# Kernel optimization log

Measured on AMD Instinct MI355X. Metric: run time of the kernel, lower is better.

Reference implementation:

```python
import jax, jax.numpy as jnp
import numpy as np

NEG_SLOPE = 0.2

def _gat_conv(x, src, dst, W, att_src, att_dst, bias, num_nodes):
    # x: [N, Fin], W: [H*C, Fin], att_*: [H, C], bias: [H*C]
    H, C = att_src.shape
    xh = (x @ W.T).reshape(num_nodes, H, C)            # [N,H,C]
    a_s = jnp.einsum('nhc,hc->nh', xh, att_src)         # [N,H]
    a_d = jnp.einsum('nhc,hc->nh', xh, att_dst)
    e = jax.nn.leaky_relu(a_s[src] + a_d[dst], NEG_SLOPE)  # [E,H]
    # segment softmax over destination node per head
    m = jax.ops.segment_max(e, dst, num_segments=num_nodes)      # [N,H]
    ex = jnp.exp(e - m[dst])
    s = jax.ops.segment_sum(ex, dst, num_segments=num_nodes)     # [N,H]
    alpha = ex / (s[dst] + 1e-16)                                # [E,H]
    msg = xh[src] * alpha[:, :, None]                            # [E,H,C]
    out = jax.ops.segment_sum(msg, dst, num_segments=num_nodes)  # [N,H,C]
    return out.reshape(num_nodes, H * C) + bias


def setup_inputs() -> dict:
    key = jax.random.key(0)
    ks = jax.random.split(key, 16)
    N, E, Fin, Hd, H1, G = 50000, 800000, 128, 128, 4, 128
    x = jax.random.normal(ks[0], (N, Fin), dtype=jnp.float32)
    edge_index = jax.random.randint(ks[1], (2, E), 0, N, dtype=jnp.int64)
    batch = jnp.sort(jax.random.randint(ks[2], (N,), 0, G, dtype=jnp.int64))
    sc1 = 1.0 / np.sqrt(Fin)
    sc2 = 1.0 / np.sqrt(Hd * H1)
    sch = 1.0 / np.sqrt(Hd)
    return {
        'x': x, 'edge_index': edge_index, 'batch': batch,
        'W1': jax.random.normal(ks[3], (Hd * H1, Fin), dtype=jnp.float32) * sc1,
        'as1': jax.random.normal(ks[4], (H1, Hd), dtype=jnp.float32) * 0.1,
        'ad1': jax.random.normal(ks[5], (H1, Hd), dtype=jnp.float32) * 0.1,
        'b1': jnp.zeros((Hd * H1,), dtype=jnp.float32),
        'W2': jax.random.normal(ks[6], (Hd, Hd * H1), dtype=jnp.float32) * sc2,
        'as2': jax.random.normal(ks[7], (1, Hd), dtype=jnp.float32) * 0.1,
        'ad2': jax.random.normal(ks[8], (1, Hd), dtype=jnp.float32) * 0.1,
        'b2': jnp.zeros((Hd,), dtype=jnp.float32),
        'Wh1': jax.random.normal(ks[9], (Hd, Hd), dtype=jnp.float32) * sch,
        'bh1': jnp.zeros((Hd,), dtype=jnp.float32),
        'Wh2': jax.random.normal(ks[10], (1, Hd), dtype=jnp.float32) * sch,
        'bh2': jnp.zeros((1,), dtype=jnp.float32),
    }


def reference(x, edge_index, batch, W1, as1, ad1, b1, W2, as2, ad2, b2, Wh1, bh1, Wh2, bh2):
    N = x.shape[0]
    G = 128  # num graphs
    # add self loops (PyG GATConv default)
    loops = jnp.arange(N, dtype=edge_index.dtype)
    src = jnp.concatenate([edge_index[0], loops])
    dst = jnp.concatenate([edge_index[1], loops])
    h = _gat_conv(x, src, dst, W1, as1, ad1, b1, N)   # [N, 512]
    h = jax.nn.elu(h)
    h = _gat_conv(h, src, dst, W2, as2, ad2, b2, N)   # [N, 128]
    h = jax.nn.elu(h)
    # global mean pool over batch
    sums = jax.ops.segment_sum(h, batch, num_segments=G)
    cnts = jax.ops.segment_sum(jnp.ones((N,), dtype=h.dtype), batch, num_segments=G)
    pooled = sums / jnp.maximum(cnts, 1.0)[:, None]   # [G, 128]
    z = jax.nn.relu(pooled @ Wh1.T + bh1)
    out = z @ Wh2.T + bh2                             # [G, 1]
    return out.reshape(-1)
```

## Files before the change

### kernel.cpp

```cpp
#include <hip/hip_runtime.h>
#include <cstdint>
#include <cstddef>

#define NEG_SLOPE 0.2f

typedef _Float16 f16x8 __attribute__((ext_vector_type(8)));
typedef _Float16 f16x2 __attribute__((ext_vector_type(2)));
typedef float    f32x4 __attribute__((ext_vector_type(4)));
typedef float    f32x2 __attribute__((ext_vector_type(2)));

__device__ __forceinline__ float leaky(float x){ return x > 0.f ? x : NEG_SLOPE * x; }
__device__ __forceinline__ float elu(float x){ return x > 0.f ? x : __expf(x) - 1.f; }

__global__ __launch_bounds__(256) void k_prep(const float* __restrict__ W1,
                                              const float* __restrict__ W2,
                                              const float* __restrict__ as1,
                                              const float* __restrict__ ad1,
                                              _Float16* __restrict__ W1hi, _Float16* __restrict__ W1lo,
                                              _Float16* __restrict__ W2hi, _Float16* __restrict__ W2lo,
                                              float* __restrict__ w_s, float* __restrict__ w_d)
{
    int b = blockIdx.x;
    if (b < 512) {
        const float* src = (b < 256) ? W1 : W2;
        _Float16* hi = (b < 256) ? W1hi : W2hi;
        _Float16* lo = (b < 256) ? W1lo : W2lo;
        int i = ((b & 255) << 8) + threadIdx.x;
        float v = src[i];
        _Float16 h = (_Float16)v;
        hi[i] = h;
        lo[i] = (_Float16)(v - (float)h);
    } else {
        int h = (b - 512) * 2 + (threadIdx.x >> 7);
        int k = threadIdx.x & 127;
        float s = 0.f, d = 0.f;
        for (int c = 0; c < 128; ++c) {
            float w = W1[((size_t)(h * 128 + c)) * 128 + k];
            s += as1[h * 128 + c] * w;
            d += ad1[h * 128 + c] * w;
        }
        w_s[h * 128 + k] = s;
        w_d[h * 128 + k] = d;
    }
}

#define LSG 40
#define CP  136
template<bool FUSE_BIAS_ELU, bool FUSE_ATTN2>
__global__ __launch_bounds__(256, 2) void k_gemm_h(
    const _Float16* __restrict__ A, const _Float16* __restrict__ Bh,
    const _Float16* __restrict__ Bl, const float* __restrict__ bias,
    _Float16* __restrict__ C,
    const float* __restrict__ as2, const float* __restrict__ ad2,
    float* __restrict__ As2, float* __restrict__ Ad2,
    int M, int K, int lda, int ldb, int ldc,
    long aZ, long bZ, long cZ, long biasZ)
{
    __shared__ __align__(16) _Float16 smem[128 * CP];
    _Float16* As  = smem;
    _Float16* Bhs = smem + 128 * LSG;
    _Float16* Bls = smem + 256 * LSG;

    const _Float16* Ab  = A  + (size_t)blockIdx.z * aZ;
    const _Float16* Bhb = Bh + (size_t)blockIdx.z * bZ;
    const _Float16* Blb = Bl + (size_t)blockIdx.z * bZ;
    _Float16* Cb = C + (size_t)blockIdx.z * cZ;

    const int tid = threadIdx.x;
    const int wave = tid >> 6, lane = tid & 63;
    const int wm = wave >> 1, wn = wave & 1;
    const int quad = lane >> 4, l16 = lane & 15;
    const int m0 = blockIdx.x * 128;

    f32x4 acc[4][4] = {};

    for (int k0 = 0; k0 < K; k0 += 32) {
// ... 42 lines not shown
                if (FUSE_BIAS_ELU) v = elu(v + bb);
                smem[(wm * 64 + i * 16 + quad * 4 + r) * CP + n] = (_Float16)v;
            }
    }
    __syncthreads();
    for (int c = tid; c < 2048; c += 256) {
        int row = c >> 4, col8 = (c & 15) * 8;
        int m = m0 + row;
        if (m < M)
            *(f16x8*)(Cb + (size_t)m * ldc + col8) = *(const f16x8*)&smem[row * CP + col8];
    }
    if (FUSE_ATTN2) {
        int row = tid >> 1, half = tid & 1;
        int d = m0 + row;
        float ss = 0.f, sd = 0.f;
        const _Float16* rp = &smem[row * CP + half * 64];
        #pragma unroll
        for (int c8 = 0; c8 < 8; ++c8) {
            f16x8 v = *(const f16x8*)(rp + c8 * 8);
            #pragma unroll
            for (int c = 0; c < 8; ++c) {
                float f = (float)v[c];
                int n = half * 64 + c8 * 8 + c;
                ss += f * as2[n];
                sd += f * ad2[n];
            }
        }
        ss += __shfl_xor(ss, 1);
        sd += __shfl_xor(sd, 1);
        if (half == 0 && d < M) { As2[d] = ss; Ad2[d] = sd; }
    }
}

__global__ __launch_bounds__(256) void k_attn_x(const float* __restrict__ x,
                                                const float* __restrict__ w_s,
                                                const float* __restrict__ w_d,
                                                float* __restrict__ a_s,
                                                float* __restrict__ a_d,
                                                _Float16* __restrict__ xh, int N)
{
    int n = blockIdx.x * 4 + (threadIdx.x >> 6);
    if (n >= N) return;
    int lane = threadIdx.x & 63;
    float2 xv = *(const float2*)(x + (size_t)n * 128 + lane * 2);
    f16x2 hv = { (_Float16)xv.x, (_Float16)xv.y };
    *(f16x2*)(xh + (size_t)n * 128 + lane * 2) = hv;
    float ps[4], pd[4];
    #pragma unroll
    for (int h = 0; h < 4; ++h) {
        float2 sv = *(const float2*)(w_s + h * 128 + lane * 2);
        float2 dv = *(const float2*)(w_d + h * 128 + lane * 2);
        ps[h] = xv.x * sv.x + xv.y * sv.y;
        pd[h] = xv.x * dv.x + xv.y * dv.y;
    }
    #pragma unroll
    for (int h = 0; h < 4; ++h)
        for (int off = 32; off; off >>= 1) {
            ps[h] += __shfl_xor(ps[h], off);
            pd[h] += __shfl_xor(pd[h], off);
        }
    if (lane == 0) {
        *(float4*)(a_s + (size_t)n * 4) = make_float4(ps[0], ps[1], ps[2], ps[3]);
        *(float4*)(a_d + (size_t)n * 4) = make_float4(pd[0], pd[1], pd[2], pd[3]);
    }
}

__global__ void k_count(const int* __restrict__ ei, int* __restrict__ deg,
                        unsigned short* __restrict__ rank,
                        const int* __restrict__ batch, int* __restrict__ gstart,
                        int E, int Ep, int N, int G, int nbc)
{
    if ((int)blockIdx.x < nbc) {
        int e = blockIdx.x * 256 + threadIdx.x;
        if (e >= Ep) return;
        int dst = (e < E) ? ei[E + e] : (e - E);
        rank[e] = (unsigned short)atomicAdd(&deg[dst], 1);
    } else {
        int n = (blockIdx.x - nbc) * 256 + threadIdx.x;
        if (n >= N) return;
        int b = batch[n];
        int prev = (n == 0) ? -1 : batch[n - 1];
        for (int g = prev + 1; g <= b; ++g) gstart[g] = n;
        if (n == N - 1)
            for (int g = b + 1; g <= G; ++g) gstart[g] = N;
    }
}

__global__ __launch_bounds__(1024) void k_scanA(const int* __restrict__ deg,
                                                int* __restrict__ start,
                                                int* __restrict__ sums, int Ntot, int N)
{
    __shared__ int sm[1024];
    int tid = threadIdx.x;
    int i = blockIdx.x * 1024 + tid;
    int v = (i < N) ? deg[i] : 0;
    sm[tid] = v; __syncthreads();
    for (int off = 1; off < 1024; off <<= 1) {
        int t = (tid >= off) ? sm[tid - off] : 0;
        __syncthreads();
        sm[tid] += t;
        __syncthreads();
    }
    if (i < Ntot) start[i] = sm[tid] - v;
    if (tid == 1023) sums[blockIdx.x] = sm[1023];
}

__global__ void k_scanB(int* sums, int nb)
{
    int l = threadIdx.x;
    int v = (l < nb) ? sums[l] : 0;
    int orig = v;
    for (int off = 1; off < 64; off <<= 1) { int t = __shfl_up(v, off); if (l >= off) v += t; }
    if (l < nb) sums[l] = v - orig;
}

__global__ __launch_bounds__(1024) void k_scanC(int* __restrict__ start,
                                                const int* __restrict__ sums, int Ntot)
{
    int i = blockIdx.x * 1024 + threadIdx.x;
    if (i < Ntot) start[i] += sums[blockIdx.x];
}

__global__ void k_fill(const int* __restrict__ ei, const int* __restrict__ start,
                       const unsigned short* __restrict__ rank,
                       unsigned short* __restrict__ csr_src, int E, int Ep)
{
    int e = blockIdx.x * blockDim.x + threadIdx.x;
    if (e >= Ep) return;
    int src, dst;
    if (e < E) { src = ei[e]; dst = ei[E + e]; } else { src = dst = e - E; }
    csr_src[start[dst] + rank[e]] = (unsigned short)src;
}

__global__ __launch_bounds__(256) void k_gat1(const int* __restrict__ start,
                                              const unsigned short* __restrict__ csr,
                                              const float* __restrict__ a_s,
                                              const float* __restrict__ a_d,
                                              const _Float16* __restrict__ x,
                                              _Float16* __restrict__ agg, int N)
{
    int d = blockIdx.x * 16 + (threadIdx.x >> 4);
    if (d >= N) return;
    int g16 = threadIdx.x & 15;
    int beg = start[d], end = start[d + 1];
    int deg = end - beg;
    float4 ad4 = *(const float4*)(a_d + (size_t)d * 4);

    float sum0 = 0.f, sum1 = 0.f, sum2 = 0.f, sum3 = 0.f;
    f32x2 acc[4][4] = {};
    const _Float16* xb = x + g16 * 8;

    for (int base = 0; base < deg; base += 16) {
        int nch = deg - base; if (nch > 16) nch = 16;
        int s = 0;
        float e0 = 0.f, e1 = 0.f, e2 = 0.f, e3 = 0.f;
        if (g16 < nch) {
            s = csr[beg + base + g16];
            float4 as4 = *(const float4*)(a_s + (size_t)s * 4);
            e0 = __expf(leaky(as4.x + ad4.x));
            e1 = __expf(leaky(as4.y + ad4.y));
            e2 = __expf(leaky(as4.z + ad4.z));
            e3 = __expf(leaky(as4.w + ad4.w));
            sum0 += e0; sum1 += e1; sum2 += e2; sum3 += e3;
        }
        int t = 0;
        for (; t + 4 <= nch; t += 4) {
            int sA = __shfl(s, t, 16),     sB = __shfl(s, t + 1, 16);
            int sC = __shfl(s, t + 2, 16), sD = __shfl(s, t + 3, 16);
            f16x8 hA = *(const f16x8*)(xb + (size_t)sA * 128);
            f16x8 hB = *(const f16x8*)(xb + (size_t)sB * 128);
            f16x8 hC = *(const f16x8*)(xb + (size_t)sC * 128);
            f16x8 hD = *(const f16x8*)(xb + (size_t)sD * 128);
            float w0A = __shfl(e0, t, 16),     w1A = __shfl(e1, t, 16);
            float w2A = __shfl(e2, t, 16),     w3A = __shfl(e3, t, 16);
            float w0B = __shfl(e0, t + 1, 16), w1B = __shfl(e1, t + 1, 16);
            float w2B = __shfl(e2, t + 1, 16), w3B = __shfl(e3, t + 1, 16);
            float w0C = __shfl(e0, t + 2, 16), w1C = __shfl(e1, t + 2, 16);
            float w2C = __shfl(e2, t + 2, 16), w3C = __shfl(e3, t + 2, 16);
            float w0D = __shfl(e0, t + 3, 16), w1D = __shfl(e1, t + 3, 16);
            float w2D = __shfl(e2, t + 3, 16), w3D = __shfl(e3, t + 3, 16);
            #pragma unroll
            for (int p = 0; p < 4; ++p) {
                f32x2 vA = { (float)hA[2*p], (float)hA[2*p+1] };
                f32x2 vB = { (float)hB[2*p], (float)hB[2*p+1] };
                f32x2 vC = { (float)hC[2*p], (float)hC[2*p+1] };
                f32x2 vD = { (float)hD[2*p], (float)hD[2*p+1] };
                acc[0][p] += w0A * vA + w0B * vB + w0C * vC + w0D * vD;
                acc[1][p] += w1A * vA + w1B * vB + w1C * vC + w1D * vD;
                acc[2][p] += w2A * vA + w2B * vB + w2C * vC + w2D * vD;
                acc[3][p] += w3A * vA + w3B * vB + w3C * vC + w3D * vD;
            }
        }
        for (; t < nch; ++t) {
            int   si = __shfl(s,  t, 16);
            float w0 = __shfl(e0, t, 16);
            float w1 = __shfl(e1, t, 16);
            float w2 = __shfl(e2, t, 16);
            float w3 = __shfl(e3, t, 16);
            f16x8 hv = *(const f16x8*)(xb + (size_t)si * 128);
            #pragma unroll
            for (int p = 0; p < 4; ++p) {
                f32x2 v = { (float)hv[2*p], (float)hv[2*p+1] };
                acc[0][p] += w0 * v;
                acc[1][p] += w1 * v;
                acc[2][p] += w2 * v;
                acc[3][p] += w3 * v;
            }
        }
    }
    #pragma unroll
    for (int o = 1; o < 16; o <<= 1) {
        sum0 += __shfl_xor(sum0, o, 16); sum1 += __shfl_xor(sum1, o, 16);
        sum2 += __shfl_xor(sum2, o, 16); sum3 += __shfl_xor(sum3, o, 16);
    }
    float inv[4] = { 1.f / (sum0 + 1e-16f), 1.f / (sum1 + 1e-16f),
                     1.f / (sum2 + 1e-16f), 1.f / (sum3 + 1e-16f) };
    _Float16* o = agg + (size_t)d * 512 + g16 * 8;
    #pragma unroll
    for (int h = 0; h < 4; ++h) {
        f16x8 ov;
        #pragma unroll
        for (int p = 0; p < 4; ++p) {
            ov[2 * p]     = (_Float16)(acc[h][p].x * inv[h]);
            ov[2 * p + 1] = (_Float16)(acc[h][p].y * inv[h]);
        }
        *(f16x8*)(o + h * 128) = ov;
    }
}

__global__ __launch_bounds__(256) void k_gat2(const int* __restrict__ start,
                                              const unsigned short* __restrict__ csr,
                                              const float* __restrict__ a_s,
                                              const float* __restrict__ a_d,
                                              const _Float16* __restrict__ xh2,
                                              const float* __restrict__ b2,
                                              _Float16* __restrict__ h2, int N)
{
    int d = blockIdx.x * 16 + (threadIdx.x >> 4);
    if (d >= N) return;
    int g16 = threadIdx.x & 15;
    int beg = start[d], end = start[d + 1];
    int deg = end - beg;
    float ad = a_d[d];

    float sum = 0.f;
    f32x2 acc[4] = {};
    const _Float16* xb = xh2 + g16 * 8;

    for (int base = 0; base < deg; base += 16) {
        int nch = deg - base; if (nch > 16) nch = 16;
        int s = 0; float e = 0.f;
        if (g16 < nch) {
            s = csr[beg + base + g16];
            e = __expf(leaky(a_s[s] + ad));
            sum += e;
        }
        int t = 0;
        for (; t + 4 <= nch; t += 4) {
            int sA = __shfl(s, t, 16),     sB = __shfl(s, t + 1, 16);
            int sC = __shfl(s, t + 2, 16), sD = __shfl(s, t + 3, 16);
            f16x8 hA = *(const f16x8*)(xb + (size_t)sA * 128);
            f16x8 hB = *(const f16x8*)(xb + (size_t)sB * 128);
            f16x8 hC = *(const f16x8*)(xb + (size_t)sC * 128);
            f16x8 hD = *(const f16x8*)(xb + (size_t)sD * 128);
            float wA = __shfl(e, t, 16),     wB = __shfl(e, t + 1, 16);
            float wC = __shfl(e, t + 2, 16), wD = __shfl(e, t + 3, 16);
            #pragma unroll
            for (int p = 0; p < 4; ++p) {
                f32x2 vA = { (float)hA[2*p], (float)hA[2*p+1] };
                f32x2 vB = { (float)hB[2*p], (float)hB[2*p+1] };
                f32x2 vC = { (float)hC[2*p], (float)hC[2*p+1] };
                f32x2 vD = { (float)hD[2*p], (float)hD[2*p+1] };
                acc[p] += wA * vA + wB * vB + wC * vC + wD * vD;
            }
        }
        for (; t < nch; ++t) {
            int   si = __shfl(s, t, 16);
            float w  = __shfl(e, t, 16);
            f16x8 hv = *(const f16x8*)(xb + (size_t)si * 128);
            #pragma unroll
            for (int p = 0; p < 4; ++p) {
                f32x2 v = { (float)hv[2*p], (float)hv[2*p+1] };
                acc[p] += w * v;
            }
        }
    }
    #pragma unroll
    for (int o = 1; o < 16; o <<= 1) sum += __shfl_xor(sum, o, 16);
    float inv = 1.f / (sum + 1e-16f);
    f16x8 ov;
    #pragma unroll
    for (int p = 0; p < 4; ++p) {
        ov[2 * p]     = (_Float16)elu(acc[p].x * inv + b2[g16 * 8 + 2 * p]);
        ov[2 * p + 1] = (_Float16)elu(acc[p].y * inv + b2[g16 * 8 + 2 * p + 1]);
    }
    *(f16x8*)(h2 + (size_t)d * 128 + g16 * 8) = ov;
}

#define PCH 64
__global__ __launch_bounds__(128) void k_poolA(const _Float16* __restrict__ h2,
                                               const int* __restrict__ batch,
                                               float* __restrict__ pooled, int N)
{
    int c = threadIdx.x;
    int n0 = blockIdx.x * PCH;
    int n1 = n0 + PCH < N ? n0 + PCH : N;
    if (n0 >= N) return;
    int g = batch[n0];
    float acc = 0.f;
    for (int n = n0; n < n1; ++n) {
        int bg = batch[n];
        if (bg != g) { atomicAdd(&pooled[(size_t)g * 128 + c], acc); acc = 0.f; g = bg; }
        acc += (float)h2[(size_t)n * 128 + c];
    }
    atomicAdd(&pooled[(size_t)g * 128 + c], acc);
}

__global__ __launch_bounds__(128) void k_head(const float* __restrict__ pooled,
                                              const int* __restrict__ gstart,
                                              const float* __restrict__ Wh1,
                                              const float* __restrict__ bh1,
                                              const float* __restrict__ Wh2,
                                              const float* __restrict__ bh2,
                                              float* __restrict__ out)
{
    int g = blockIdx.x, c = threadIdx.x;
    __shared__ float p[128];
    __shared__ float red[128];
    float cf = (float)(gstart[g + 1] - gstart[g]); cf = cf > 1.f ? cf : 1.f;
    p[c] = pooled[(size_t)g * 128 + c] / cf;
    __syncthreads();
    float z = bh1[c];
    for (int k = 0; k < 128; ++k) z += p[k] * Wh1[c * 128 + k];
    z = z > 0.f ? z : 0.f;
    red[c] = z * Wh2[c];
    __syncthreads();
    for (int st = 64; st > 0; st >>= 1) { if (c < st) red[c] += red[c + st]; __syncthreads(); }
    if (c == 0) out[g] = red[0] + bh2[0];
}

extern "C" void kernel_launch(void* const* d_in, const int* in_sizes, int n_in,
                              void* d_out, int out_size, void* d_ws, size_t ws_size,
                              hipStream_t stream)
{
    const float* x   = (const float*)d_in[0];
    const int*   ei  = (const int*)d_in[1];
    const int*   bat = (const int*)d_in[2];
    const float* W1  = (const float*)d_in[3];
    const float* as1 = (const float*)d_in[4];
    const float* ad1 = (const float*)d_in[5];
    const float* b1  = (const float*)d_in[6];
    const float* W2  = (const float*)d_in[7];
    const float* as2 = (const float*)d_in[8];
    const float* ad2 = (const float*)d_in[9];
    const float* b2  = (const float*)d_in[10];
    const float* Wh1 = (const float*)d_in[11];
    const float* bh1 = (const float*)d_in[12];
    const float* Wh2 = (const float*)d_in[13];
    const float* bh2 = (const float*)d_in[14];
    float* out = (float*)d_out;

    const int N  = in_sizes[0] / 128;
    const int E  = in_sizes[1] / 2;
    const int Ep = E + N;
    const int G  = 128;

    char* w = (char*)d_ws;
    size_t off = 0;
    auto alloc = [&](size_t bytes) -> char* {
        char* p = w + off; off += (bytes + 511) & ~(size_t)511; return p;
    };
    _Float16* x_h  = (_Float16*)alloc((size_t)N * 128 * 2);
    _Float16* agg  = (_Float16*)alloc((size_t)N * 512 * 2);
    _Float16* h1   = (_Float16*)alloc((size_t)N * 512 * 2);
    _Float16* xh2h = (_Float16*)alloc((size_t)N * 128 * 2);
    _Float16* h2   = (_Float16*)alloc((size_t)N * 128 * 2);
    float*    As1  = (float*)alloc((size_t)N * 4 * 4);
    float*    Ad1  = (float*)alloc((size_t)N * 4 * 4);
    float*    As2  = (float*)alloc((size_t)N * 4);
    float*    Ad2  = (float*)alloc((size_t)N * 4);
    float*    w_s1 = (float*)alloc(512 * 4);
    float*    w_d1 = (float*)alloc(512 * 4);
    _Float16* W1hi = (_Float16*)alloc(65536 * 2);
    _Float16* W1lo = (_Float16*)alloc(65536 * 2);
    _Float16* W2hi = (_Float16*)alloc(65536 * 2);
    _Float16* W2lo = (_Float16*)alloc(65536 * 2);
    int* startb = (int*)alloc((size_t)(N + 1) * 4);
    unsigned short* csr  = (unsigned short*)alloc((size_t)Ep * 2);
    unsigned short* rank = (unsigned short*)alloc((size_t)Ep * 2);
    int* sums   = (int*)alloc(4096);
    int* gstart = (int*)alloc((size_t)(G + 1) * 4);
    char* zbase = w + off;
    int*   deg    = (int*)alloc((size_t)N * 4);
    float* pooled = (float*)alloc((size_t)G * 128 * 4);
    size_t zbytes = (size_t)((w + off) - zbase);

    hipMemsetAsync(zbase, 0, zbytes, stream);

    k_prep<<<514, 256, 0, stream>>>(W1, W2, as1, ad1, W1hi, W1lo, W2hi, W2lo, w_s1, w_d1);
    k_attn_x<<<(N + 3) / 4, 256, 0, stream>>>(x, w_s1, w_d1, As1, Ad1, x_h, N);
    int nbc = (Ep + 255) / 256, nbg = (N + 255) / 256;
    k_count<<<nbc + nbg, 256, 0, stream>>>(ei, deg, rank, bat, gstart, E, Ep, N, G, nbc);
    int nb = (N + 1 + 1023) / 1024;
    k_scanA<<<nb, 1024, 0, stream>>>(deg, startb, sums, N + 1, N);
    k_scanB<<<1, 64, 0, stream>>>(sums, nb);
    k_scanC<<<nb, 1024, 0, stream>>>(startb, sums, N + 1);
    k_fill<<<(Ep + 255) / 256, 256, 0, stream>>>(ei, startb, rank, csr, E, Ep);
    k_gat1<<<(N + 15) / 16, 256, 0, stream>>>(startb, csr, As1, Ad1, x_h, agg, N);
    k_gemm_h<true, false><<<dim3((N + 127) / 128, 1, 4), 256, 0, stream>>>(
        agg, W1hi, W1lo, b1, h1, nullptr, nullptr, nullptr, nullptr,
        N, 128, 512, 128, 512, 128L, 16384L, 128L, 128L);
    k_gemm_h<false, true><<<dim3((N + 127) / 128, 1, 1), 256, 0, stream>>>(
        h1, W2hi, W2lo, nullptr, xh2h, as2, ad2, As2, Ad2,
        N, 512, 512, 512, 128, 0L, 0L, 0L, 0L);
    k_gat2<<<(N + 15) / 16, 256, 0, stream>>>(startb, csr, As2, Ad2, xh2h, b2, h2, N);
    k_poolA<<<(N + PCH - 1) / PCH, 128, 0, stream>>>(h2, bat, pooled, N);
    k_head<<<G, 128, 0, stream>>>(pooled, gstart, Wh1, bh1, Wh2, bh2, out);
}
```

Baseline: 346.9 us.

## Fuse layer-1 GEMM into GAT1 aggregation and pooling into GAT2

The layer-1 aggregation kernel now stages its 16 aggregated rows in shared memory and multiplies them directly by the per-head W1 hi/lo splits with MFMA, applying bias and ELU before writing h1. This removes the agg buffer round trip and one GEMM launch. Separately, GAT2 now applies ELU and atomically adds each node's output into the per-graph pooled sums, dropping the h2 buffer and the pooling kernel. The costs are that every block re-reads W1 from cache with little reuse (16 rows per block), and that the pooling step now issues per-element float atomics on only 128 graph rows, which can contend heavily.

```diff
diff --git a/kernel.cpp b/kernel.cpp
--- a/kernel.cpp
+++ b/kernel.cpp
@@ -250,99 +250,139 @@
     csr_src[start[dst] + rank[e]] = (unsigned short)src;
 }
 
+#define ATP 520
 __global__ __launch_bounds__(256) void k_gat1(const int* __restrict__ start,
                                               const unsigned short* __restrict__ csr,
                                               const float* __restrict__ a_s,
                                               const float* __restrict__ a_d,
                                               const _Float16* __restrict__ x,
-                                              _Float16* __restrict__ agg, int N)
-{
-    int d = blockIdx.x * 16 + (threadIdx.x >> 4);
-    if (d >= N) return;
-    int g16 = threadIdx.x & 15;
-    int beg = start[d], end = start[d + 1];
-    int deg = end - beg;
-    float4 ad4 = *(const float4*)(a_d + (size_t)d * 4);
-
-    float sum0 = 0.f, sum1 = 0.f, sum2 = 0.f, sum3 = 0.f;
-    f32x2 acc[4][4] = {};
-    const _Float16* xb = x + g16 * 8;
-
-    for (int base = 0; base < deg; base += 16) {
-        int nch = deg - base; if (nch > 16) nch = 16;
-        int s = 0;
-        float e0 = 0.f, e1 = 0.f, e2 = 0.f, e3 = 0.f;
-        if (g16 < nch) {
-            s = csr[beg + base + g16];
-            float4 as4 = *(const float4*)(a_s + (size_t)s * 4);
-            e0 = __expf(leaky(as4.x + ad4.x));
-            e1 = __expf(leaky(as4.y + ad4.y));
-            e2 = __expf(leaky(as4.z + ad4.z));
-            e3 = __expf(leaky(as4.w + ad4.w));
-            sum0 += e0; sum1 += e1; sum2 += e2; sum3 += e3;
-        }
-        int t = 0;
-        for (; t + 4 <= nch; t += 4) {
-            int sA = __shfl(s, t, 16),     sB = __shfl(s, t + 1, 16);
-            int sC = __shfl(s, t + 2, 16), sD = __shfl(s, t + 3, 16);
-            f16x8 hA = *(const f16x8*)(xb + (size_t)sA * 128);
-            f16x8 hB = *(const f16x8*)(xb + (size_t)sB * 128);
-            f16x8 hC = *(const f16x8*)(xb + (size_t)sC * 128);
-            f16x8 hD = *(const f16x8*)(xb + (size_t)sD * 128);
-            float w0A = __shfl(e0, t, 16),     w1A = __shfl(e1, t, 16);
-            float w2A = __shfl(e2, t, 16),     w3A = __shfl(e3, t, 16);
-            float w0B = __shfl(e0, t + 1, 16), w1B = __shfl(e1, t + 1, 16);
-            float w2B = __shfl(e2, t + 1, 16), w3B = __shfl(e3, t + 1, 16);
-            float w0C = __shfl(e0, t + 2, 16), w1C = __shfl(e1, t + 2, 16);
-            float w2C = __shfl(e2, t + 2, 16), w3C = __shfl(e3, t + 2, 16);
-            float w0D = __shfl(e0, t + 3, 16), w1D = __shfl(e1, t + 3, 16);
-            float w2D = __shfl(e2, t + 3, 16), w3D = __shfl(e3, t + 3, 16);
+                                              const _Float16* __restrict__ W1hi,
+                                              const _Float16* __restrict__ W1lo,
+                                              const float* __restrict__ b1,
+                                              _Float16* __restrict__ h1, int N)
+{
+    __shared__ __align__(16) _Float16 At[16 * ATP];
+    const int grp = threadIdx.x >> 4;
+    const int g16 = threadIdx.x & 15;
+    const int d = blockIdx.x * 16 + grp;
+
+    if (d < N) {
+        int beg = start[d], end = start[d + 1];
+        int deg = end - beg;
+        float4 ad4 = *(const float4*)(a_d + (size_t)d * 4);
+
+        float sum0 = 0.f, sum1 = 0.f, sum2 = 0.f, sum3 = 0.f;
+        f32x2 acc[4][4] = {};
+        const _Float16* xb = x + g16 * 8;
+
+        for (int base = 0; base < deg; base += 16) {
+            int nch = deg - base; if (nch > 16) nch = 16;
+            int s = 0;
+            float e0 = 0.f, e1 = 0.f, e2 = 0.f, e3 = 0.f;
+            if (g16 < nch) {
+                s = csr[beg + base + g16];
+                float4 as4 = *(const float4*)(a_s + (size_t)s * 4);
+                e0 = __expf(leaky(as4.x + ad4.x));
+                e1 = __expf(leaky(as4.y + ad4.y));
+                e2 = __expf(leaky(as4.z + ad4.z));
+                e3 = __expf(leaky(as4.w + ad4.w));
+                sum0 += e0; sum1 += e1; sum2 += e2; sum3 += e3;
+            }
+            int t = 0;
+            for (; t + 4 <= nch; t += 4) {
+                int sA = __shfl(s, t, 16),     sB = __shfl(s, t + 1, 16);
+                int sC = __shfl(s, t + 2, 16), sD = __shfl(s, t + 3, 16);
+                f16x8 hA = *(const f16x8*)(xb + (size_t)sA * 128);
+                f16x8 hB = *(const f16x8*)(xb + (size_t)sB * 128);
+                f16x8 hC = *(const f16x8*)(xb + (size_t)sC * 128);
+                f16x8 hD = *(const f16x8*)(xb + (size_t)sD * 128);
+                float w0A = __shfl(e0, t, 16),     w1A = __shfl(e1, t, 16);
+                float w2A = __shfl(e2, t, 16),     w3A = __shfl(e3, t, 16);
+                float w0B = __shfl(e0, t + 1, 16), w1B = __shfl(e1, t + 1, 16);
+                float w2B = __shfl(e2, t + 1, 16), w3B = __shfl(e3, t + 1, 16);
+                float w0C = __shfl(e0, t + 2, 16), w1C = __shfl(e1, t + 2, 16);
+                float w2C = __shfl(e2, t + 2, 16), w3C = __shfl(e3, t + 2, 16);
+                float w0D = __shfl(e0, t + 3, 16), w1D = __shfl(e1, t + 3, 16);
+                float w2D = __shfl(e2, t + 3, 16), w3D = __shfl(e3, t + 3, 16);
+                #pragma unroll
+                for (int p = 0; p < 4; ++p) {
+                    f32x2 vA = { (float)hA[2*p], (float)hA[2*p+1] };
+                    f32x2 vB = { (float)hB[2*p], (float)hB[2*p+1] };
+                    f32x2 vC = { (float)hC[2*p], (float)hC[2*p+1] };
+                    f32x2 vD = { (float)hD[2*p], (float)hD[2*p+1] };
+                    acc[0][p] += w0A * vA + w0B * vB + w0C * vC + w0D * vD;
+                    acc[1][p] += w1A * vA + w1B * vB + w1C * vC + w1D * vD;
+                    acc[2][p] += w2A * vA + w2B * vB + w2C * vC + w2D * vD;
+                    acc[3][p] += w3A * vA + w3B * vB + w3C * vC + w3D * vD;
+                }
+            }
+            for (; t < nch; ++t) {
+                int   si = __shfl(s,  t, 16);
+                float w0 = __shfl(e0, t, 16);
+                float w1 = __shfl(e1, t, 16);
+                float w2 = __shfl(e2, t, 16);
+                float w3 = __shfl(e3, t, 16);
+                f16x8 hv = *(const f16x8*)(xb + (size_t)si * 128);
+                #pragma unroll
+                for (int p = 0; p < 4; ++p) {
+                    f32x2 v = { (float)hv[2*p], (float)hv[2*p+1] };
+                    acc[0][p] += w0 * v;
+                    acc[1][p] += w1 * v;
+                    acc[2][p] += w2 * v;
+                    acc[3][p] += w3 * v;
+                }
+            }
+        }
+        #pragma unroll
+        for (int o = 1; o < 16; o <<= 1) {
+            sum0 += __shfl_xor(sum0, o, 16); sum1 += __shfl_xor(sum1, o, 16);
+            sum2 += __shfl_xor(sum2, o, 16); sum3 += __shfl_xor(sum3, o, 16);
+        }
+        float inv[4] = { 1.f / (sum0 + 1e-16f), 1.f / (sum1 + 1e-16f),
+                         1.f / (sum2 + 1e-16f), 1.f / (sum3 + 1e-16f) };
+        _Float16* o = At + grp * ATP + g16 * 8;
+        #pragma unroll
+        for (int h = 0; h < 4; ++h) {
+            f16x8 ov;
             #pragma unroll
             for (int p = 0; p < 4; ++p) {
-                f32x2 vA = { (float)hA[2*p], (float)hA[2*p+1] };
-                f32x2 vB = { (float)hB[2*p], (float)hB[2*p+1] };
-                f32x2 vC = { (float)hC[2*p], (float)hC[2*p+1] };
-                f32x2 vD = { (float)hD[2*p], (float)hD[2*p+1] };
-                acc[0][p] += w0A * vA + w0B * vB + w0C * vC + w0D * vD;
-                acc[1][p] += w1A * vA + w1B * vB + w1C * vC + w1D * vD;
-                acc[2][p] += w2A * vA + w2B * vB + w2C * vC + w2D * vD;
-                acc[3][p] += w3A * vA + w3B * vB + w3C * vC + w3D * vD;
-            }
-        }
-        for (; t < nch; ++t) {
-            int   si = __shfl(s,  t, 16);
-            float w0 = __shfl(e0, t, 16);
-            float w1 = __shfl(e1, t, 16);
-            float w2 = __shfl(e2, t, 16);
-            float w3 = __shfl(e3, t, 16);
-            f16x8 hv = *(const f16x8*)(xb + (size_t)si * 128);
-            #pragma unroll
-            for (int p = 0; p < 4; ++p) {
-                f32x2 v = { (float)hv[2*p], (float)hv[2*p+1] };
-                acc[0][p] += w0 * v;
-                acc[1][p] += w1 * v;
-                acc[2][p] += w2 * v;
-                acc[3][p] += w3 * v;
-            }
-        }
-    }
-    #pragma unroll
-    for (int o = 1; o < 16; o <<= 1) {
-        sum0 += __shfl_xor(sum0, o, 16); sum1 += __shfl_xor(sum1, o, 16);
-        sum2 += __shfl_xor(sum2, o, 16); sum3 += __shfl_xor(sum3, o, 16);
-    }
-    float inv[4] = { 1.f / (sum0 + 1e-16f), 1.f / (sum1 + 1e-16f),
-                     1.f / (sum2 + 1e-16f), 1.f / (sum3 + 1e-16f) };
-    _Float16* o = agg + (size_t)d * 512 + g16 * 8;
-    #pragma unroll
-    for (int h = 0; h < 4; ++h) {
-        f16x8 ov;
-        #pragma unroll
-        for (int p = 0; p < 4; ++p) {
-            ov[2 * p]     = (_Float16)(acc[h][p].x * inv[h]);
-            ov[2 * p + 1] = (_Float16)(acc[h][p].y * inv[h]);
-        }
-        *(f16x8*)(o + h * 128) = ov;
+                ov[2 * p]     = (_Float16)(acc[h][p].x * inv[h]);
+                ov[2 * p + 1] = (_Float16)(acc[h][p].y * inv[h]);
+            }
+            *(f16x8*)(o + h * 128) = ov;
+        }
+    }
+    __syncthreads();
+
+    const int wave = threadIdx.x >> 6, lane = threadIdx.x & 63;
+    const int quad = lane >> 4, l16 = lane & 15;
+    const int m0 = blockIdx.x * 16;
+
+    f16x8 af[4];
+    #pragma unroll
+    for (int k0 = 0; k0 < 4; ++k0)
+        af[k0] = *(const f16x8*)&At[l16 * ATP + wave * 128 + k0 * 32 + quad * 8];
+
+    #pragma unroll
+    for (int nt = 0; nt < 8; ++nt) {
+        const size_t brow = ((size_t)(wave * 128 + nt * 16 + l16)) * 128 + quad * 8;
+        const _Float16* bh = W1hi + brow;
+        const _Float16* bl = W1lo + brow;
+        f32x4 c = {};
+        #pragma unroll
+        for (int k0 = 0; k0 < 4; ++k0) {
+            f16x8 vh = *(const f16x8*)(bh + k0 * 32);
+            f16x8 vl = *(const f16x8*)(bl + k0 * 32);
+            c = __builtin_amdgcn_mfma_f32_16x16x32_f16(af[k0], vh, c, 0, 0, 0);
+            c = __builtin_amdgcn_mfma_f32_16x16x32_f16(af[k0], vl, c, 0, 0, 0);
+        }
+        float bb = b1[wave * 128 + nt * 16 + l16];
+        #pragma unroll
+        for (int r = 0; r < 4; ++r) {
+            int m = quad * 4 + r;
+            if (m0 + m < N)
+                h1[(size_t)(m0 + m) * 512 + wave * 128 + nt * 16 + l16] = (_Float16)elu(c[r] + bb);
+        }
     }
 }
 
@@ -352,7 +392,8 @@
                                               const float* __restrict__ a_d,
                                               const _Float16* __restrict__ xh2,
                                               const float* __restrict__ b2,
-                                              _Float16* __restrict__ h2, int N)
+                                              const int* __restrict__ batch,
+                                              float* __restrict__ pooled, int N)
 {
     int d = blockIdx.x * 16 + (threadIdx.x >> 4);
     if (d >= N) return;
@@ -406,32 +447,12 @@
     #pragma unroll
     for (int o = 1; o < 16; o <<= 1) sum += __shfl_xor(sum, o, 16);
     float inv = 1.f / (sum + 1e-16f);
-    f16x8 ov;
+    float* pg = pooled + (size_t)batch[d] * 128 + g16 * 8;
     #pragma unroll
     for (int p = 0; p < 4; ++p) {
-        ov[2 * p]     = (_Float16)elu(acc[p].x * inv + b2[g16 * 8 + 2 * p]);
-        ov[2 * p + 1] = (_Float16)elu(acc[p].y * inv + b2[g16 * 8 + 2 * p + 1]);
-    }
-    *(f16x8*)(h2 + (size_t)d * 128 + g16 * 8) = ov;
-}
-
-#define PCH 64
-__global__ __launch_bounds__(128) void k_poolA(const _Float16* __restrict__ h2,
-                                               const int* __restrict__ batch,
-                                               float* __restrict__ pooled, int N)
-{
-    int c = threadIdx.x;
-    int n0 = blockIdx.x * PCH;
-    int n1 = n0 + PCH < N ? n0 + PCH : N;
-    if (n0 >= N) return;
-    int g = batch[n0];
-    float acc = 0.f;
-    for (int n = n0; n < n1; ++n) {
-        int bg = batch[n];
-        if (bg != g) { atomicAdd(&pooled[(size_t)g * 128 + c], acc); acc = 0.f; g = bg; }
-        acc += (float)h2[(size_t)n * 128 + c];
-    }
-    atomicAdd(&pooled[(size_t)g * 128 + c], acc);
+        atomicAdd(&pg[2 * p],     elu(acc[p].x * inv + b2[g16 * 8 + 2 * p]));
+        atomicAdd(&pg[2 * p + 1], elu(acc[p].y * inv + b2[g16 * 8 + 2 * p + 1]));
+    }
 }
 
 __global__ __launch_bounds__(128) void k_head(const float* __restrict__ pooled,
@@ -489,10 +510,8 @@
         char* p = w + off; off += (bytes + 511) & ~(size_t)511; return p;
     };
     _Float16* x_h  = (_Float16*)alloc((size_t)N * 128 * 2);
-    _Float16* agg  = (_Float16*)alloc((size_t)N * 512 * 2);
     _Float16* h1   = (_Float16*)alloc((size_t)N * 512 * 2);
     _Float16* xh2h = (_Float16*)alloc((size_t)N * 128 * 2);
-    _Float16* h2   = (_Float16*)alloc((size_t)N * 128 * 2);
     float*    As1  = (float*)alloc((size_t)N * 4 * 4);
     float*    Ad1  = (float*)alloc((size_t)N * 4 * 4);
     float*    As2  = (float*)alloc((size_t)N * 4);
@@ -524,14 +543,11 @@
     k_scanB<<<1, 64, 0, stream>>>(sums, nb);
     k_scanC<<<nb, 1024, 0, stream>>>(startb, sums, N + 1);
     k_fill<<<(Ep + 255) / 256, 256, 0, stream>>>(ei, startb, rank, csr, E, Ep);
-    k_gat1<<<(N + 15) / 16, 256, 0, stream>>>(startb, csr, As1, Ad1, x_h, agg, N);
-    k_gemm_h<true, false><<<dim3((N + 127) / 128, 1, 4), 256, 0, stream>>>(
-        agg, W1hi, W1lo, b1, h1, nullptr, nullptr, nullptr, nullptr,
-        N, 128, 512, 128, 512, 128L, 16384L, 128L, 128L);
+    k_gat1<<<(N + 15) / 16, 256, 0, stream>>>(startb, csr, As1, Ad1, x_h,
+                                              W1hi, W1lo, b1, h1, N);
     k_gemm_h<false, true><<<dim3((N + 127) / 128, 1, 1), 256, 0, stream>>>(
         h1, W2hi, W2lo, nullptr, xh2h, as2, ad2, As2, Ad2,
         N, 512, 512, 512, 128, 0L, 0L, 0L, 0L);
-    k_gat2<<<(N + 15) / 16, 256, 0, stream>>>(startb, csr, As2, Ad2, xh2h, b2, h2, N);
-    k_poolA<<<(N + PCH - 1) / PCH, 128, 0, stream>>>(h2, bat, pooled, N);
+    k_gat2<<<(N + 15) / 16, 256, 0, stream>>>(startb, csr, As2, Ad2, xh2h, b2, bat, pooled, N);
     k_head<<<G, 128, 0, stream>>>(pooled, gstart, Wh1, bh1, Wh2, bh2, out);
 }
```

After: 654.4 us. 1.89x slower.

## Merge front-end kernels and split GAT gathers into two half-width passes

Applied to the files above, without the earlier changes.

Fuses weight prep, degree counting and graph-start computation into one launch, and fuses the block scan with the attention-logit kernel. The separate scanB launch is dropped by having scanC sum the preceding block totals itself. The gat1/gat2 aggregation kernels now gather 8-byte f16x4 slices in two passes over the neighbour list, unrolled eight deep. This lowers register pressure and adds memory-level parallelism, but it reads the CSR and recomputes the exponentials twice. The goal is less launch overhead and better latency hiding in the gather kernels.

```diff
diff --git a/kernel.cpp b/kernel.cpp
--- a/kernel.cpp
+++ b/kernel.cpp
@@ -5,6 +5,7 @@
 #define NEG_SLOPE 0.2f
 
 typedef _Float16 f16x8 __attribute__((ext_vector_type(8)));
+typedef _Float16 f16x4 __attribute__((ext_vector_type(4)));
 typedef _Float16 f16x2 __attribute__((ext_vector_type(2)));
 typedef float    f32x4 __attribute__((ext_vector_type(4)));
 typedef float    f32x2 __attribute__((ext_vector_type(2)));
@@ -12,13 +13,17 @@
 __device__ __forceinline__ float leaky(float x){ return x > 0.f ? x : NEG_SLOPE * x; }
 __device__ __forceinline__ float elu(float x){ return x > 0.f ? x : __expf(x) - 1.f; }
 
-__global__ __launch_bounds__(256) void k_prep(const float* __restrict__ W1,
-                                              const float* __restrict__ W2,
-                                              const float* __restrict__ as1,
-                                              const float* __restrict__ ad1,
-                                              _Float16* __restrict__ W1hi, _Float16* __restrict__ W1lo,
-                                              _Float16* __restrict__ W2hi, _Float16* __restrict__ W2lo,
-                                              float* __restrict__ w_s, float* __restrict__ w_d)
+__global__ __launch_bounds__(256) void k_front(const float* __restrict__ W1,
+                                               const float* __restrict__ W2,
+                                               const float* __restrict__ as1,
+                                               const float* __restrict__ ad1,
+                                               _Float16* __restrict__ W1hi, _Float16* __restrict__ W1lo,
+                                               _Float16* __restrict__ W2hi, _Float16* __restrict__ W2lo,
+                                               float* __restrict__ w_s, float* __restrict__ w_d,
+                                               const int* __restrict__ ei, int* __restrict__ deg,
+                                               unsigned short* __restrict__ rank,
+                                               const int* __restrict__ batch, int* __restrict__ gstart,
+                                               int E, int Ep, int N, int G, int nbc)
 {
     int b = blockIdx.x;
     if (b < 512) {
@@ -30,7 +35,7 @@
         _Float16 h = (_Float16)v;
         hi[i] = h;
         lo[i] = (_Float16)(v - (float)h);
-    } else {
+    } else if (b < 514) {
         int h = (b - 512) * 2 + (threadIdx.x >> 7);
         int k = threadIdx.x & 127;
         float s = 0.f, d = 0.f;
@@ -41,7 +46,93 @@
         }
         w_s[h * 128 + k] = s;
         w_d[h * 128 + k] = d;
-    }
+    } else if (b < 514 + nbc) {
+        int e = (b - 514) * 256 + threadIdx.x;
+        if (e >= Ep) return;
+        int dst = (e < E) ? ei[E + e] : (e - E);
+        rank[e] = (unsigned short)atomicAdd(&deg[dst], 1);
+    } else {
+        int n = (b - 514 - nbc) * 256 + threadIdx.x;
+        if (n >= N) return;
+        int bb = batch[n];
+        int prev = (n == 0) ? -1 : batch[n - 1];
+        for (int g = prev + 1; g <= bb; ++g) gstart[g] = n;
+        if (n == N - 1)
+            for (int g = bb + 1; g <= G; ++g) gstart[g] = N;
+    }
+}
+
+__global__ __launch_bounds__(1024) void k_scan_attn(const int* __restrict__ deg,
+                                                    int* __restrict__ start,
+                                                    int* __restrict__ sums,
+                                                    int Ntot, int N, int nscan,
+                                                    const float* __restrict__ x,
+                                                    const float* __restrict__ w_s,
+                                                    const float* __restrict__ w_d,
+                                                    float* __restrict__ a_s,
+                                                    float* __restrict__ a_d,
+                                                    _Float16* __restrict__ xh)
+{
+    if ((int)blockIdx.x < nscan) {
+        __shared__ int sm[1024];
+        int tid = threadIdx.x;
+        int i = blockIdx.x * 1024 + tid;
+        int v = (i < N) ? deg[i] : 0;
+        sm[tid] = v; __syncthreads();
+        for (int off = 1; off < 1024; off <<= 1) {
+            int t = (tid >= off) ? sm[tid - off] : 0;
+            __syncthreads();
+            sm[tid] += t;
+            __syncthreads();
+        }
+        if (i < Ntot) start[i] = sm[tid] - v;
+        if (tid == 1023) sums[blockIdx.x] = sm[1023];
+    } else {
+        int n = (blockIdx.x - nscan) * 16 + (threadIdx.x >> 6);
+        if (n >= N) return;
+        int lane = threadIdx.x & 63;
+        float2 xv = *(const float2*)(x + (size_t)n * 128 + lane * 2);
+        f16x2 hv = { (_Float16)xv.x, (_Float16)xv.y };
+        *(f16x2*)(xh + (size_t)n * 128 + lane * 2) = hv;
+        float ps[4], pd[4];
+        #pragma unroll
+        for (int h = 0; h < 4; ++h) {
+            float2 sv = *(const float2*)(w_s + h * 128 + lane * 2);
+            float2 dv = *(const float2*)(w_d + h * 128 + lane * 2);
+            ps[h] = xv.x * sv.x + xv.y * sv.y;
+            pd[h] = xv.x * dv.x + xv.y * dv.y;
+        }
+        #pragma unroll
+        for (int h = 0; h < 4; ++h)
+            for (int off = 32; off; off >>= 1) {
+                ps[h] += __shfl_xor(ps[h], off);
+                pd[h] += __shfl_xor(pd[h], off);
+            }
+        if (lane == 0) {
+            *(float4*)(a_s + (size_t)n * 4) = make_float4(ps[0], ps[1], ps[2], ps[3]);
+            *(float4*)(a_d + (size_t)n * 4) = make_float4(pd[0], pd[1], pd[2], pd[3]);
+        }
+    }
+}
+
+__global__ __launch_bounds__(1024) void k_scanC(int* __restrict__ start,
+                                                const int* __restrict__ sums, int Ntot)
+{
+    int add = 0;
+    for (int b = 0; b < (int)blockIdx.x; ++b) add += sums[b];
+    int i = blockIdx.x * 1024 + threadIdx.x;
+    if (i < Ntot) start[i] += add;
+}
+
+__global__ void k_fill(const int* __restrict__ ei, const int* __restrict__ start,
+                       const unsigned short* __restrict__ rank,
+                       unsigned short* __restrict__ csr_src, int E, int Ep)
+{
+    int e = blockIdx.x * blockDim.x + threadIdx.x;
+    if (e >= Ep) return;
+    int src, dst;
+    if (e < E) { src = ei[e]; dst = ei[E + e]; } else { src = dst = e - E; }
+    csr_src[start[dst] + rank[e]] = (unsigned short)src;
 }
 
 #define LSG 40
@@ -150,106 +241,6 @@
     }
 }
 
-__global__ __launch_bounds__(256) void k_attn_x(const float* __restrict__ x,
-                                                const float* __restrict__ w_s,
-                                                const float* __restrict__ w_d,
-                                                float* __restrict__ a_s,
-                                                float* __restrict__ a_d,
-                                                _Float16* __restrict__ xh, int N)
-{
-    int n = blockIdx.x * 4 + (threadIdx.x >> 6);
-    if (n >= N) return;
-    int lane = threadIdx.x & 63;
-    float2 xv = *(const float2*)(x + (size_t)n * 128 + lane * 2);
-    f16x2 hv = { (_Float16)xv.x, (_Float16)xv.y };
-    *(f16x2*)(xh + (size_t)n * 128 + lane * 2) = hv;
-    float ps[4], pd[4];
-    #pragma unroll
-    for (int h = 0; h < 4; ++h) {
-        float2 sv = *(const float2*)(w_s + h * 128 + lane * 2);
-        float2 dv = *(const float2*)(w_d + h * 128 + lane * 2);
-        ps[h] = xv.x * sv.x + xv.y * sv.y;
-        pd[h] = xv.x * dv.x + xv.y * dv.y;
-    }
-    #pragma unroll
-    for (int h = 0; h < 4; ++h)
-        for (int off = 32; off; off >>= 1) {
-            ps[h] += __shfl_xor(ps[h], off);
-            pd[h] += __shfl_xor(pd[h], off);
-        }
-    if (lane == 0) {
-        *(float4*)(a_s + (size_t)n * 4) = make_float4(ps[0], ps[1], ps[2], ps[3]);
-        *(float4*)(a_d + (size_t)n * 4) = make_float4(pd[0], pd[1], pd[2], pd[3]);
-    }
-}
-
-__global__ void k_count(const int* __restrict__ ei, int* __restrict__ deg,
-                        unsigned short* __restrict__ rank,
-                        const int* __restrict__ batch, int* __restrict__ gstart,
-                        int E, int Ep, int N, int G, int nbc)
-{
-    if ((int)blockIdx.x < nbc) {
-        int e = blockIdx.x * 256 + threadIdx.x;
-        if (e >= Ep) return;
-        int dst = (e < E) ? ei[E + e] : (e - E);
-        rank[e] = (unsigned short)atomicAdd(&deg[dst], 1);
-    } else {
-        int n = (blockIdx.x - nbc) * 256 + threadIdx.x;
-        if (n >= N) return;
-        int b = batch[n];
-        int prev = (n == 0) ? -1 : batch[n - 1];
-        for (int g = prev + 1; g <= b; ++g) gstart[g] = n;
-        if (n == N - 1)
-            for (int g = b + 1; g <= G; ++g) gstart[g] = N;
-    }
-}
-
-__global__ __launch_bounds__(1024) void k_scanA(const int* __restrict__ deg,
-                                                int* __restrict__ start,
-                                                int* __restrict__ sums, int Ntot, int N)
-{
-    __shared__ int sm[1024];
-    int tid = threadIdx.x;
-    int i = blockIdx.x * 1024 + tid;
-    int v = (i < N) ? deg[i] : 0;
-    sm[tid] = v; __syncthreads();
-    for (int off = 1; off < 1024; off <<= 1) {
-        int t = (tid >= off) ? sm[tid - off] : 0;
-        __syncthreads();
-        sm[tid] += t;
-        __syncthreads();
-    }
-    if (i < Ntot) start[i] = sm[tid] - v;
-    if (tid == 1023) sums[blockIdx.x] = sm[1023];
-}
-
-__global__ void k_scanB(int* sums, int nb)
-{
-    int l = threadIdx.x;
-    int v = (l < nb) ? sums[l] : 0;
-    int orig = v;
-    for (int off = 1; off < 64; off <<= 1) { int t = __shfl_up(v, off); if (l >= off) v += t; }
-    if (l < nb) sums[l] = v - orig;
-}
-
-__global__ __launch_bounds__(1024) void k_scanC(int* __restrict__ start,
-                                                const int* __restrict__ sums, int Ntot)
-{
-    int i = blockIdx.x * 1024 + threadIdx.x;
-    if (i < Ntot) start[i] += sums[blockIdx.x];
-}
-
-__global__ void k_fill(const int* __restrict__ ei, const int* __restrict__ start,
-                       const unsigned short* __restrict__ rank,
-                       unsigned short* __restrict__ csr_src, int E, int Ep)
-{
-    int e = blockIdx.x * blockDim.x + threadIdx.x;
-    if (e >= Ep) return;
-    int src, dst;
-    if (e < E) { src = ei[e]; dst = ei[E + e]; } else { src = dst = e - E; }
-    csr_src[start[dst] + rank[e]] = (unsigned short)src;
-}
-
 __global__ __launch_bounds__(256) void k_gat1(const int* __restrict__ start,
                                               const unsigned short* __restrict__ csr,
                                               const float* __restrict__ a_s,
@@ -263,86 +254,75 @@
     int beg = start[d], end = start[d + 1];
     int deg = end - beg;
     float4 ad4 = *(const float4*)(a_d + (size_t)d * 4);
-
-    float sum0 = 0.f, sum1 = 0.f, sum2 = 0.f, sum3 = 0.f;
-    f32x2 acc[4][4] = {};
-    const _Float16* xb = x + g16 * 8;
-
-    for (int base = 0; base < deg; base += 16) {
-        int nch = deg - base; if (nch > 16) nch = 16;
-        int s = 0;
-        float e0 = 0.f, e1 = 0.f, e2 = 0.f, e3 = 0.f;
-        if (g16 < nch) {
-            s = csr[beg + base + g16];
-            float4 as4 = *(const float4*)(a_s + (size_t)s * 4);
-            e0 = __expf(leaky(as4.x + ad4.x));
-            e1 = __expf(leaky(as4.y + ad4.y));
-            e2 = __expf(leaky(as4.z + ad4.z));
-            e3 = __expf(leaky(as4.w + ad4.w));
-            sum0 += e0; sum1 += e1; sum2 += e2; sum3 += e3;
-        }
-        int t = 0;
-        for (; t + 4 <= nch; t += 4) {
-            int sA = __shfl(s, t, 16),     sB = __shfl(s, t + 1, 16);
-            int sC = __shfl(s, t + 2, 16), sD = __shfl(s, t + 3, 16);
-            f16x8 hA = *(const f16x8*)(xb + (size_t)sA * 128);
-            f16x8 hB = *(const f16x8*)(xb + (size_t)sB * 128);
-            f16x8 hC = *(const f16x8*)(xb + (size_t)sC * 128);
-            f16x8 hD = *(const f16x8*)(xb + (size_t)sD * 128);
-            float w0A = __shfl(e0, t, 16),     w1A = __shfl(e1, t, 16);
-            float w2A = __shfl(e2, t, 16),     w3A = __shfl(e3, t, 16);
-            float w0B = __shfl(e0, t + 1, 16), w1B = __shfl(e1, t + 1, 16);
-            float w2B = __shfl(e2, t + 1, 16), w3B = __shfl(e3, t + 1, 16);
-            float w0C = __shfl(e0, t + 2, 16), w1C = __shfl(e1, t + 2, 16);
-            float w2C = __shfl(e2, t + 2, 16), w3C = __shfl(e3, t + 2, 16);
-            float w0D = __shfl(e0, t + 3, 16), w1D = __shfl(e1, t + 3, 16);
-            float w2D = __shfl(e2, t + 3, 16), w3D = __shfl(e3, t + 3, 16);
+    float inv0 = 0.f, inv1 = 0.f, inv2 = 0.f, inv3 = 0.f;
+
+    #pragma unroll
+    for (int half = 0; half < 2; ++half) {
+        f32x4 acc0 = {}, acc1 = {}, acc2 = {}, acc3 = {};
+        float sum0 = 0.f, sum1 = 0.f, sum2 = 0.f, sum3 = 0.f;
+        const _Float16* xb = x + half * 64 + g16 * 4;
+
+        for (int base = 0; base < deg; base += 16) {
+            int nch = deg - base; if (nch > 16) nch = 16;
+            int s = 0;
+            float e0 = 0.f, e1 = 0.f, e2 = 0.f, e3 = 0.f;
+            if (g16 < nch) {
+                s = csr[beg + base + g16];
+                float4 as4 = *(const float4*)(a_s + (size_t)s * 4);
+                e0 = __expf(leaky(as4.x + ad4.x));
+                e1 = __expf(leaky(as4.y + ad4.y));
+                e2 = __expf(leaky(as4.z + ad4.z));
+                e3 = __expf(leaky(as4.w + ad4.w));
+                if (half == 0) { sum0 += e0; sum1 += e1; sum2 += e2; sum3 += e3; }
+            }
+            int t = 0;
+            for (; t + 8 <= nch; t += 8) {
+                int si[8];
+                #pragma unroll
+                for (int u = 0; u < 8; ++u) si[u] = __shfl(s, t + u, 16);
+                f16x4 hv[8];
+                #pragma unroll
+                for (int u = 0; u < 8; ++u) hv[u] = *(const f16x4*)(xb + (size_t)si[u] * 128);
+                #pragma unroll
+                for (int u = 0; u < 8; ++u) {
+                    float w0 = __shfl(e0, t + u, 16), w1 = __shfl(e1, t + u, 16);
+                    float w2 = __shfl(e2, t + u, 16), w3 = __shfl(e3, t + u, 16);
+                    f32x4 v = { (float)hv[u][0], (float)hv[u][1], (float)hv[u][2], (float)hv[u][3] };
+                    acc0 += w0 * v; acc1 += w1 * v; acc2 += w2 * v; acc3 += w3 * v;
+                }
+            }
+            for (; t < nch; ++t) {
+                int   si = __shfl(s,  t, 16);
+                float w0 = __shfl(e0, t, 16), w1 = __shfl(e1, t, 16);
+                float w2 = __shfl(e2, t, 16), w3 = __shfl(e3, t, 16);
+                f16x4 hv = *(const f16x4*)(xb + (size_t)si * 128);
+                f32x4 v = { (float)hv[0], (float)hv[1], (float)hv[2], (float)hv[3] };
+                acc0 += w0 * v; acc1 += w1 * v; acc2 += w2 * v; acc3 += w3 * v;
+            }
+        }
+        if (half == 0) {
             #pragma unroll
-            for (int p = 0; p < 4; ++p) {
-                f32x2 vA = { (float)hA[2*p], (float)hA[2*p+1] };
-                f32x2 vB = { (float)hB[2*p], (float)hB[2*p+1] };
-                f32x2 vC = { (float)hC[2*p], (float)hC[2*p+1] };
-                f32x2 vD = { (float)hD[2*p], (float)hD[2*p+1] };
-                acc[0][p] += w0A * vA + w0B * vB + w0C * vC + w0D * vD;
-                acc[1][p] += w1A * vA + w1B * vB + w1C * vC + w1D * vD;
-                acc[2][p] += w2A * vA + w2B * vB + w2C * vC + w2D * vD;
-                acc[3][p] += w3A * vA + w3B * vB + w3C * vC + w3D * vD;
-            }
-        }
-        for (; t < nch; ++t) {
-            int   si = __shfl(s,  t, 16);
-            float w0 = __shfl(e0, t, 16);
-            float w1 = __shfl(e1, t, 16);
-            float w2 = __shfl(e2, t, 16);
-            float w3 = __shfl(e3, t, 16);
-            f16x8 hv = *(const f16x8*)(xb + (size_t)si * 128);
-            #pragma unroll
-            for (int p = 0; p < 4; ++p) {
-                f32x2 v = { (float)hv[2*p], (float)hv[2*p+1] };
-                acc[0][p] += w0 * v;
-                acc[1][p] += w1 * v;
-                acc[2][p] += w2 * v;
-                acc[3][p] += w3 * v;
-            }
-        }
-    }
-    #pragma unroll
-    for (int o = 1; o < 16; o <<= 1) {
-        sum0 += __shfl_xor(sum0, o, 16); sum1 += __shfl_xor(sum1, o, 16);
-        sum2 += __shfl_xor(sum2, o, 16); sum3 += __shfl_xor(sum3, o, 16);
-    }
-    float inv[4] = { 1.f / (sum0 + 1e-16f), 1.f / (sum1 + 1e-16f),
-                     1.f / (sum2 + 1e-16f), 1.f / (sum3 + 1e-16f) };
-    _Float16* o = agg + (size_t)d * 512 + g16 * 8;
-    #pragma unroll
-    for (int h = 0; h < 4; ++h) {
-        f16x8 ov;
-        #pragma unroll
-        for (int p = 0; p < 4; ++p) {
-            ov[2 * p]     = (_Float16)(acc[h][p].x * inv[h]);
-            ov[2 * p + 1] = (_Float16)(acc[h][p].y * inv[h]);
-        }
-        *(f16x8*)(o + h * 128) = ov;
+            for (int o = 1; o < 16; o <<= 1) {
+                sum0 += __shfl_xor(sum0, o, 16); sum1 += __shfl_xor(sum1, o, 16);
+                sum2 += __shfl_xor(sum2, o, 16); sum3 += __shfl_xor(sum3, o, 16);
+            }
+            inv0 = 1.f / (sum0 + 1e-16f); inv1 = 1.f / (sum1 + 1e-16f);
+            inv2 = 1.f / (sum2 + 1e-16f); inv3 = 1.f / (sum3 + 1e-16f);
+        }
+        _Float16* o = agg + (size_t)d * 512 + half * 64 + g16 * 4;
+        f16x4 ov;
+        #pragma unroll
+        for (int j = 0; j < 4; ++j) ov[j] = (_Float16)(acc0[j] * inv0);
+        *(f16x4*)(o)       = ov;
+        #pragma unroll
+        for (int j = 0; j < 4; ++j) ov[j] = (_Float16)(acc1[j] * inv1);
+        *(f16x4*)(o + 128) = ov;
+        #pragma unroll
+        for (int j = 0; j < 4; ++j) ov[j] = (_Float16)(acc2[j] * inv2);
+        *(f16x4*)(o + 256) = ov;
+        #pragma unroll
+        for (int j = 0; j < 4; ++j) ov[j] = (_Float16)(acc3[j] * inv3);
+        *(f16x4*)(o + 384) = ov;
     }
 }
 
@@ -360,59 +340,56 @@
     int beg = start[d], end = start[d + 1];
     int deg = end - beg;
     float ad = a_d[d];
-
-    float sum = 0.f;
-    f32x2 acc[4] = {};
-    const _Float16* xb = xh2 + g16 * 8;
-
-    for (int base = 0; base < deg; base += 16) {
-        int nch = deg - base; if (nch > 16) nch = 16;
-        int s = 0; float e = 0.f;
-        if (g16 < nch) {
-            s = csr[beg + base + g16];
-            e = __expf(leaky(a_s[s] + ad));
-            sum += e;
-        }
-        int t = 0;
-        for (; t + 4 <= nch; t += 4) {
-            int sA = __shfl(s, t, 16),     sB = __shfl(s, t + 1, 16);
-            int sC = __shfl(s, t + 2, 16), sD = __shfl(s, t + 3, 16);
-            f16x8 hA = *(const f16x8*)(xb + (size_t)sA * 128);
-            f16x8 hB = *(const f16x8*)(xb + (size_t)sB * 128);
-            f16x8 hC = *(const f16x8*)(xb + (size_t)sC * 128);
-            f16x8 hD = *(const f16x8*)(xb + (size_t)sD * 128);
-            float wA = __shfl(e, t, 16),     wB = __shfl(e, t + 1, 16);
-            float wC = __shfl(e, t + 2, 16), wD = __shfl(e, t + 3, 16);
+    float inv = 0.f;
+
+    #pragma unroll
+    for (int half = 0; half < 2; ++half) {
+        f32x4 acc = {};
+        float sum = 0.f;
+        const _Float16* xb = xh2 + half * 64 + g16 * 4;
+
+        for (int base = 0; base < deg; base += 16) {
+            int nch = deg - base; if (nch > 16) nch = 16;
+            int s = 0; float e = 0.f;
+            if (g16 < nch) {
+                s = csr[beg + base + g16];
+                e = __expf(leaky(a_s[s] + ad));
+                if (half == 0) sum += e;
+            }
+            int t = 0;
+            for (; t + 8 <= nch; t += 8) {
+                int si[8];
+                #pragma unroll
+                for (int u = 0; u < 8; ++u) si[u] = __shfl(s, t + u, 16);
+                f16x4 hv[8];
+                #pragma unroll
+                for (int u = 0; u < 8; ++u) hv[u] = *(const f16x4*)(xb + (size_t)si[u] * 128);
+                #pragma unroll
+                for (int u = 0; u < 8; ++u) {
+                    float w = __shfl(e, t + u, 16);
+                    f32x4 v = { (float)hv[u][0], (float)hv[u][1], (float)hv[u][2], (float)hv[u][3] };
+                    acc += w * v;
+                }
+            }
+            for (; t < nch; ++t) {
+                int   si = __shfl(s, t, 16);
+                float w  = __shfl(e, t, 16);
+                f16x4 hv = *(const f16x4*)(xb + (size_t)si * 128);
+                f32x4 v = { (float)hv[0], (float)hv[1], (float)hv[2], (float)hv[3] };
+                acc += w * v;
+            }
+        }
+        if (half == 0) {
             #pragma unroll
-            for (int p = 0; p < 4; ++p) {
-                f32x2 vA = { (float)hA[2*p], (float)hA[2*p+1] };
-                f32x2 vB = { (float)hB[2*p], (float)hB[2*p+1] };
-                f32x2 vC = { (float)hC[2*p], (float)hC[2*p+1] };
-                f32x2 vD = { (float)hD[2*p], (float)hD[2*p+1] };
-                acc[p] += wA * vA + wB * vB + wC * vC + wD * vD;
-            }
-        }
-        for (; t < nch; ++t) {
-            int   si = __shfl(s, t, 16);
-            float w  = __shfl(e, t, 16);
-            f16x8 hv = *(const f16x8*)(xb + (size_t)si * 128);
-            #pragma unroll
-            for (int p = 0; p < 4; ++p) {
-                f32x2 v = { (float)hv[2*p], (float)hv[2*p+1] };
-                acc[p] += w * v;
-            }
-        }
-    }
-    #pragma unroll
-    for (int o = 1; o < 16; o <<= 1) sum += __shfl_xor(sum, o, 16);
-    float inv = 1.f / (sum + 1e-16f);
-    f16x8 ov;
-    #pragma unroll
-    for (int p = 0; p < 4; ++p) {
-        ov[2 * p]     = (_Float16)elu(acc[p].x * inv + b2[g16 * 8 + 2 * p]);
-        ov[2 * p + 1] = (_Float16)elu(acc[p].y * inv + b2[g16 * 8 + 2 * p + 1]);
-    }
-    *(f16x8*)(h2 + (size_t)d * 128 + g16 * 8) = ov;
+            for (int o = 1; o < 16; o <<= 1) sum += __shfl_xor(sum, o, 16);
+            inv = 1.f / (sum + 1e-16f);
+        }
+        f16x4 ov;
+        #pragma unroll
+        for (int j = 0; j < 4; ++j)
+            ov[j] = (_Float16)elu(acc[j] * inv + b2[half * 64 + g16 * 4 + j]);
+        *(f16x4*)(h2 + (size_t)d * 128 + half * 64 + g16 * 4) = ov;
+    }
 }
 
 #define PCH 64
@@ -482,6 +459,7 @@
     const int E  = in_sizes[1] / 2;
     const int Ep = E + N;
     const int G  = 128;
+    const int nscan = (N + 1 + 1023) / 1024;
 
     char* w = (char*)d_ws;
     size_t off = 0;
@@ -515,14 +493,13 @@
 
     hipMemsetAsync(zbase, 0, zbytes, stream);
 
-    k_prep<<<514, 256, 0, stream>>>(W1, W2, as1, ad1, W1hi, W1lo, W2hi, W2lo, w_s1, w_d1);
-    k_attn_x<<<(N + 3) / 4, 256, 0, stream>>>(x, w_s1, w_d1, As1, Ad1, x_h, N);
     int nbc = (Ep + 255) / 256, nbg = (N + 255) / 256;
-    k_count<<<nbc + nbg, 256, 0, stream>>>(ei, deg, rank, bat, gstart, E, Ep, N, G, nbc);
-    int nb = (N + 1 + 1023) / 1024;
-    k_scanA<<<nb, 1024, 0, stream>>>(deg, startb, sums, N + 1, N);
-    k_scanB<<<1, 64, 0, stream>>>(sums, nb);
-    k_scanC<<<nb, 1024, 0, stream>>>(startb, sums, N + 1);
+    k_front<<<514 + nbc + nbg, 256, 0, stream>>>(W1, W2, as1, ad1, W1hi, W1lo, W2hi, W2lo,
+                                                 w_s1, w_d1, ei, deg, rank, bat, gstart,
+                                                 E, Ep, N, G, nbc);
+    k_scan_attn<<<nscan + (N + 15) / 16, 1024, 0, stream>>>(deg, startb, sums, N + 1, N, nscan,
+                                                            x, w_s1, w_d1, As1, Ad1, x_h);
+    k_scanC<<<nscan, 1024, 0, stream>>>(startb, sums, N + 1);
     k_fill<<<(Ep + 255) / 256, 256, 0, stream>>>(ei, startb, rank, csr, E, Ep);
     k_gat1<<<(N + 15) / 16, 256, 0, stream>>>(startb, csr, As1, Ad1, x_h, agg, N);
     k_gemm_h<true, false><<<dim3((N + 127) / 128, 1, 4), 256, 0, stream>>>(
```

Result: slower. 371.9 us (+7.2%).
